# Performance work log

Measured on AMD Instinct MI355X. Metric: run time of the kernel, lower is better.

The kernel has to match this reference:

```python
import jax, jax.numpy as jnp
import numpy as np

B, IN, D1, H1, H2, NC = 16384, 1024, 8, 2048, 1024, 1000
C = IN // D1  # 128 channels, D=8 each
EPS = 1e-5


def _bn(x, g, b):
    # training-mode BatchNorm1d: biased variance over batch dim
    m = jnp.mean(x, axis=0)
    v = jnp.var(x, axis=0)
    return (x - m) * jax.lax.rsqrt(v + EPS) * g + b


def setup_inputs() -> dict:
    key = jax.random.key(0)
    ks = jax.random.split(key, 18)
    f = jax.random.normal
    return {
        "x": f(ks[0], (B, IN), jnp.float32),
        "norm0_g": 1.0 + 0.1 * f(ks[1], (IN,), jnp.float32),
        "norm0_b": 0.1 * f(ks[2], (IN,), jnp.float32),
        "S": f(ks[3], (C, D1, 15), jnp.float32),
        "Hm": f(ks[4], (15, 16), jnp.float32),
        "T": f(ks[5], (C, 15), jnp.float32),
        "LUT": f(ks[6], (C, 16, D1), jnp.float32),
        "W1": 0.02 * f(ks[7], (H1, IN), jnp.float32),
        "b1": 0.02 * f(ks[8], (H1,), jnp.float32),
        "norm1_g": 1.0 + 0.1 * f(ks[9], (H1,), jnp.float32),
        "norm1_b": 0.1 * f(ks[10], (H1,), jnp.float32),
        "W2": 0.02 * f(ks[11], (H2, H1), jnp.float32),
        "b2": 0.02 * f(ks[12], (H2,), jnp.float32),
        "norm2_g": 1.0 + 0.1 * f(ks[13], (H2,), jnp.float32),
        "norm2_b": 0.1 * f(ks[14], (H2,), jnp.float32),
        "W3": 0.02 * f(ks[15], (NC, H2), jnp.float32),
        "b3": 0.02 * f(ks[16], (NC,), jnp.float32),
    }


def reference(x, norm0_g, norm0_b, S, Hm, T, LUT, W1, b1,
              norm1_g, norm1_b, W2, b2, norm2_g, norm2_b, W3, b3):
    h = _bn(x, norm0_g, norm0_b)
    # --- MM block: per-channel small GEMMs + STE sign + STE argmax LUT ---
    xc = h.reshape(-1, C, D1)                          # [B, C, D]
    z = jnp.einsum('bcd,cdk->bck', xc, S) - T - 1e-4   # [B, C, 15]
    t = jnp.tanh(z)
    q = jax.lax.stop_gradient(jnp.sign(z) - t) + t     # STE sign
    logits = jnp.einsum('bck,kj->bcj', q, Hm)          # [B, C, 16]
    one_hot = jax.nn.one_hot(jnp.argmax(logits, axis=-1), 16, dtype=logits.dtype)
    sm = jax.nn.softmax(logits, axis=-1)
    oh_out = jnp.einsum('bck,ckd->bcd', one_hot, LUT)
    sm_out = jnp.einsum('bck,ckd->bcd', sm, LUT)
    v = jax.lax.stop_gradient(oh_out - sm_out) + sm_out  # STE argmax select
    v = v.reshape(-1, C * D1)                           # [B, IN]
    # --- MLP head ---
    h1 = jax.nn.relu(_bn(v @ W1.T + b1, norm1_g, norm1_b))
    h2 = jax.nn.relu(_bn(h1 @ W2.T + b2, norm2_g, norm2_b))
    logits3 = h2 @ W3.T + b3
    return jax.nn.log_softmax(logits3, axis=-1), h1
```

## Files before the change

### kernel.cpp

```cpp
#include <hip/hip_runtime.h>

typedef unsigned short u16;
typedef __attribute__((ext_vector_type(8))) short bf16x8;
typedef __attribute__((ext_vector_type(4))) float f32x4;
typedef __attribute__((ext_vector_type(4))) u16 u16x4;
typedef __attribute__((ext_vector_type(8))) u16 u16x8;

__device__ __forceinline__ u16 f2bf(float f) {
    union { float f; unsigned u; } v; v.f = f;
    unsigned u = v.u;
    unsigned r = (u + 0x7fffu + ((u >> 16) & 1u)) >> 16;
    return (u16)r;
}
__device__ __forceinline__ float bf2f(u16 u) {
    union { unsigned u; float f; } v; v.u = ((unsigned)u) << 16;
    return v.f;
}

__device__ __forceinline__ void gload16(const u16* g, u16* l) {
    __builtin_amdgcn_global_load_lds((const __attribute__((address_space(1))) void*)g,
                                     (__attribute__((address_space(3))) void*)l, 16, 0, 0);
}

#define WAITV(N) asm volatile("s_waitcnt vmcnt(" #N ")" ::: "memory")

__device__ __forceinline__ void sbar() {
    __builtin_amdgcn_sched_barrier(0);
    __builtin_amdgcn_s_barrier();
    __builtin_amdgcn_sched_barrier(0);
}

__device__ __forceinline__ void cvt4(const float* in, u16* out, int i) {
    f32x4 v = *(const f32x4*)(in + (size_t)i * 4);
    u16x4 o;
    o.x = f2bf(v.x); o.y = f2bf(v.y); o.z = f2bf(v.z); o.w = f2bf(v.w);
    *(u16x4*)(out + (size_t)i * 4) = o;
}

__global__ __launch_bounds__(256) void leaf_kernel(
    const float* __restrict__ W1, const float* __restrict__ W2, const float* __restrict__ W3,
    u16* __restrict__ W1b, u16* __restrict__ W2b, u16* __restrict__ W3b,
    const float* __restrict__ x, float* __restrict__ part0) {
    int bid = blockIdx.x;
    if (bid < 5120) {
        int i = bid * 256 + threadIdx.x;
        if (i < 524288) {
            cvt4(W1, W1b, i);
        } else if (i < 1048576) {
            cvt4(W2, W2b, i - 524288);
        } else {
            int j = i - 1048576;
            int e = j * 4;
            int row = e >> 10;
            u16x4 o;
            if (row < 1000) {
                f32x4 v = *(const f32x4*)(W3 + e);
                o.x = f2bf(v.x); o.y = f2bf(v.y); o.z = f2bf(v.z); o.w = f2bf(v.w);
            } else {
                o.x = 0; o.y = 0; o.z = 0; o.w = 0;
            }
            *(u16x4*)(W3b + e) = o;
        }
    } else {
        int by = bid - 5120;
        int col = threadIdx.x * 4;
        long base = (long)by * 32 * 1024 + col;
        f32x4 s = {0.f, 0.f, 0.f, 0.f};
        f32x4 q = {0.f, 0.f, 0.f, 0.f};
        for (int r = 0; r < 32; ++r) {
            f32x4 v = *(const f32x4*)(x + base + (long)r * 1024);
            s.x += v.x; s.y += v.y; s.z += v.z; s.w += v.w;
            q.x = fmaf(v.x, v.x, q.x); q.y = fmaf(v.y, v.y, q.y);
            q.z = fmaf(v.z, v.z, q.z); q.w = fmaf(v.w, v.w, q.w);
        }
        long o = ((long)by * 1024 + col) * 2;
        f32x4 p0 = {s.x, q.x, s.y, q.y};
        f32x4 p1 = {s.z, q.z, s.w, q.w};
        *(f32x4*)(part0 + o) = p0;
        *(f32x4*)(part0 + o + 4) = p1;
    }
}

__global__ __launch_bounds__(256) void col_stats_finalize(
    const float* __restrict__ part, int cols, int nblk, float inv_n,
    const float* __restrict__ g, const float* __restrict__ b, float* __restrict__ ab) {
    __shared__ float red[8][64];
    int cl = threadIdx.x & 31;
    int j = threadIdx.x >> 5;
    int col = blockIdx.x * 32 + cl;
    int per = nblk / 8;
    float s = 0.f, ss = 0.f;
    for (int i = 0; i < per; ++i) {
        long o = ((long)(j * per + i) * cols + col) * 2;
        s += part[o]; ss += part[o + 1];
    }
    red[j][cl * 2] = s;
    red[j][cl * 2 + 1] = ss;
    __syncthreads();
    if (threadIdx.x < 32) {
        int c = blockIdx.x * 32 + threadIdx.x;
        float fs = 0.f, fss = 0.f;
#pragma unroll
        for (int jj = 0; jj < 8; ++jj) {
            fs += red[jj][threadIdx.x * 2];
            fss += red[jj][threadIdx.x * 2 + 1];
        }
        float m = fs * inv_n;
        float var = fss * inv_n - m * m;
        float a = g[c] * rsqrtf(var + 1e-5f);
        ab[c * 2 + 0] = a;
        ab[c * 2 + 1] = b[c] - m * a;
    }
}

__global__ __launch_bounds__(256) void mm_block_kernel(
    const float* __restrict__ x, const float* __restrict__ ab0,
    const float* __restrict__ S, const float* __restrict__ Tt,
    const float* __restrict__ Hm, const float* __restrict__ LUT,
    u16* __restrict__ v) {
    __shared__ float sS[480];
    __shared__ float sT[60];
    __shared__ float sHm[240];
    __shared__ float sLUT[512];
    __shared__ float sAB[64];
    const int t = threadIdx.x;
    const int cb = blockIdx.y * 4;

    for (int i = t; i < 480; i += 256) sS[i] = S[cb * 120 + i];
    for (int i = t; i < 60; i += 256)  sT[i] = Tt[cb * 15 + i];
    for (int i = t; i < 240; i += 256) sHm[i] = Hm[i];
    for (int i = t; i < 512; i += 256) sLUT[i] = LUT[cb * 128 + i];
    for (int i = t; i < 64; i += 256)  sAB[i] = ab0[cb * 16 + i];
    __syncthreads();

    const int row = blockIdx.x * 256 + t;
    const float* xp = x + (size_t)row * 1024 + cb * 8;
    float xr[32];
#pragma unroll
    for (int i = 0; i < 8; ++i) {
        f32x4 v4 = *(const f32x4*)(xp + i * 4);
        xr[i * 4 + 0] = v4.x; xr[i * 4 + 1] = v4.y;
        xr[i * 4 + 2] = v4.z; xr[i * 4 + 3] = v4.w;
    }
    u16 ov[32];
#pragma unroll
    for (int ch = 0; ch < 4; ++ch) {
        float h[8];
#pragma unroll
        for (int d = 0; d < 8; ++d)
            h[d] = xr[ch * 8 + d] * sAB[ch * 16 + d * 2] + sAB[ch * 16 + d * 2 + 1];
        float lg[16];
#pragma unroll
        for (int j = 0; j < 16; ++j) lg[j] = 0.f;
        for (int k = 0; k < 15; ++k) {
            float a = 0.f;
#pragma unroll
            for (int d = 0; d < 8; ++d) a = fmaf(h[d], sS[ch * 120 + d * 15 + k], a);
            float z = (a - sT[ch * 15 + k]) - 1e-4f;
            float q = (z > 0.f) ? 1.f : ((z < 0.f) ? -1.f : 0.f);
#pragma unroll
            for (int j = 0; j < 16; ++j) lg[j] = fmaf(q, sHm[k * 16 + j], lg[j]);
        }
        int jb = 0; float best = lg[0];
#pragma unroll
        for (int j = 1; j < 16; ++j) { if (lg[j] > best) { best = lg[j]; jb = j; } }
#pragma unroll
        for (int d = 0; d < 8; ++d) ov[ch * 8 + d] = f2bf(sLUT[ch * 128 + jb * 8 + d]);
    }
    u16* vp = v + (size_t)row * 1024 + cb * 8;
#pragma unroll
    for (int ch = 0; ch < 4; ++ch)
        *(u16x8*)(vp + ch * 8) = *(u16x8*)&ov[ch * 8];
}

__global__ __launch_bounds__(256) void bn_relu_apply8(
    const u16* __restrict__ y, const float* __restrict__ ab, int cols, int total8,
    float* __restrict__ out_f32, u16* __restrict__ out_b16) {
    int i = blockIdx.x * 256 + threadIdx.x;
    if (i >= total8) return;
    long e = (long)i * 8;
    int col = (int)(e % cols);
    u16x8 yv = *(const u16x8*)(y + e);
    float r[8];
#pragma unroll
    for (int d = 0; d < 8; ++d)
        r[d] = fmaxf(bf2f(yv[d]) * ab[(col + d) * 2] + ab[(col + d) * 2 + 1], 0.f);
    if (out_f32) {
        f32x4 rf0 = {r[0], r[1], r[2], r[3]};
        f32x4 rf1 = {r[4], r[5], r[6], r[7]};
        *(f32x4*)(out_f32 + e) = rf0;
        *(f32x4*)(out_f32 + e + 4) = rf1;
    }
    u16x8 o;
#pragma unroll
    for (int d = 0; d < 8; ++d) o[d] = f2bf(r[d]);
    *(u16x8*)(out_b16 + e) = o;
}

#define MFMA16(a, b, c) __builtin_amdgcn_mfma_f32_16x16x32_bf16(a, b, c, 0, 0, 0)

template <bool STORE_BF16, bool DO_STATS>
__global__ __launch_bounds__(512, 2) void gemm256(
    const u16* __restrict__ A, const u16* __restrict__ Bm, void* __restrict__ Cv,
    const float* __restrict__ bias, float* __restrict__ part,
    int M, int N, int K, int ldc, int ncol) {
    extern __shared__ u16 lds[];
    const int BOFF = 32768;
    const int t = threadIdx.x, lane = t & 63, w = t >> 6;
    const int wr = w >> 2, wc = w & 3;
    const int fr = lane & 15, kg = lane >> 4;
    const int gx = gridDim.x, nwg = gx * gridDim.y;
    const int flat = blockIdx.y * gx + blockIdx.x;
    const int swz = (flat & 7) * (nwg >> 3) + (flat >> 3);
    const int bm = (swz % gx) * 256;
    const int bn = (swz / gx) * 256;
    const int NT = K >> 6;

    const int srow8 = lane >> 3;
    const int scc = (lane & 7) ^ srow8;
    const int L0 = w * 2;
    const u16* gAb = A + ((size_t)bm + L0 * 8 + srow8) * K + scc * 8;
    const u16* gBb = Bm + ((size_t)bn + L0 * 8 + srow8) * K + scc * 8;
    u16* ldsW = lds + L0 * 512 + lane * 8;

    const int s0 = (kg ^ (fr & 7)) * 8;
    const int s1 = s0 ^ 32;
    int rA[4], rB[2];
#pragma unroll
    for (int i = 0; i < 4; ++i) rA[i] = (i * 32 + wr * 16 + fr) * 64;
#pragma unroll
    for (int p = 0; p < 2; ++p) rB[p] = (p * 64 + wc * 16 + fr) * 64;

    f32x4 acc[8][4];
#pragma unroll
    for (int m = 0; m < 8; ++m)
#pragma unroll
        for (int n = 0; n < 4; ++n) acc[m][n] = (f32x4){0.f, 0.f, 0.f, 0.f};

    bf16x8 Ar[8][2], Br[2][2];

#define STG(gp, matOff, d, half, k0)                                          \
    {                                                                         \
        u16* dst_ = ldsW + (matOff) + ((d) * 2 + (half)) * 8192;              \
        const u16* src_ = (gp) + (size_t)((half) * 128) * K + (k0);           \
        gload16(src_, dst_);                                                  \
        gload16(src_ + (size_t)8 * K, dst_ + 512);                            \
    }
#define LDF(off) (*(const bf16x8*)&lds[off])

    STG(gAb, 0, 0, 0, 0);
    STG(gBb, BOFF, 0, 0, 0);
    STG(gAb, 0, 0, 1, 0);
    STG(gBb, BOFF, 0, 1, 0);

#pragma unroll 2
    for (int tt = 0; tt < NT - 1; ++tt) {
        const int d = tt & 1, dn = d ^ 1;
        const int k0n = (tt + 1) << 6;
        const int a0 = (d * 2) * 8192, a1 = (d * 2 + 1) * 8192;
        const int b0 = BOFF + a0, b1 = BOFF + a1;
        WAITV(4); sbar();
        STG(gAb, 0, dn, 0, k0n);
#pragma unroll
        for (int i = 0; i < 4; ++i) { Ar[i][0] = LDF(a0 + rA[i] + s0); Ar[i][1] = LDF(a0 + rA[i] + s1); }
#pragma unroll
        for (int p = 0; p < 2; ++p) { Br[p][0] = LDF(b0 + rB[p] + s0); Br[p][1] = LDF(b0 + rB[p] + s1); }
        __builtin_amdgcn_s_setprio(1);
#pragma unroll
        for (int i = 0; i < 4; ++i)
#pragma unroll
            for (int p = 0; p < 2; ++p) {
                acc[i][p] = MFMA16(Ar[i][0], Br[p][0], acc[i][p]);
                acc[i][p] = MFMA16(Ar[i][1], Br[p][1], acc[i][p]);
            }
        __builtin_amdgcn_s_setprio(0);
        WAITV(4); sbar();
        STG(gBb, BOFF, dn, 0, k0n);
#pragma unroll
        for (int i = 0; i < 4; ++i) { Ar[4 + i][0] = LDF(a1 + rA[i] + s0); Ar[4 + i][1] = LDF(a1 + rA[i] + s1); }
        __builtin_amdgcn_s_setprio(1);
#pragma unroll
        for (int i = 0; i < 4; ++i)
#pragma unroll
            for (int p = 0; p < 2; ++p) {
                acc[4 + i][p] = MFMA16(Ar[4 + i][0], Br[p][0], acc[4 + i][p]);
                acc[4 + i][p] = MFMA16(Ar[4 + i][1], Br[p][1], acc[4 + i][p]);
            }
        __builtin_amdgcn_s_setprio(0);
        WAITV(4); sbar();
        STG(gAb, 0, dn, 1, k0n);
#pragma unroll
        for (int p = 0; p < 2; ++p) { Br[p][0] = LDF(b1 + rB[p] + s0); Br[p][1] = LDF(b1 + rB[p] + s1); }
        __builtin_amdgcn_s_setprio(1);
#pragma unroll
        for (int i = 0; i < 4; ++i)
#pragma unroll
            for (int p = 0; p < 2; ++p) {
                acc[4 + i][2 + p] = MFMA16(Ar[4 + i][0], Br[p][0], acc[4 + i][2 + p]);
                acc[4 + i][2 + p] = MFMA16(Ar[4 + i][1], Br[p][1], acc[4 + i][2 + p]);
            }
        __builtin_amdgcn_s_setprio(0);
        STG(gBb, BOFF, dn, 1, k0n);
        __builtin_amdgcn_s_setprio(1);
#pragma unroll
        for (int i = 0; i < 4; ++i)
#pragma unroll
            for (int p = 0; p < 2; ++p) {
                acc[i][2 + p] = MFMA16(Ar[i][0], Br[p][0], acc[i][2 + p]);
                acc[i][2 + p] = MFMA16(Ar[i][1], Br[p][1], acc[i][2 + p]);
            }
        __builtin_amdgcn_s_setprio(0);
    }
    {
        const int d = (NT - 1) & 1;
        const int a0 = (d * 2) * 8192, a1 = (d * 2 + 1) * 8192;
        const int b0 = BOFF + a0, b1 = BOFF + a1;
        WAITV(4); sbar();
#pragma unroll
        for (int i = 0; i < 4; ++i) { Ar[i][0] = LDF(a0 + rA[i] + s0); Ar[i][1] = LDF(a0 + rA[i] + s1); }
#pragma unroll
        for (int p = 0; p < 2; ++p) { Br[p][0] = LDF(b0 + rB[p] + s0); Br[p][1] = LDF(b0 + rB[p] + s1); }
        __builtin_amdgcn_s_setprio(1);
#pragma unroll
        for (int i = 0; i < 4; ++i)
#pragma unroll
            for (int p = 0; p < 2; ++p) {
                acc[i][p] = MFMA16(Ar[i][0], Br[p][0], acc[i][p]);
                acc[i][p] = MFMA16(Ar[i][1], Br[p][1], acc[i][p]);
            }
        __builtin_amdgcn_s_setprio(0);
        WAITV(2); sbar();
#pragma unroll
        for (int i = 0; i < 4; ++i) { Ar[4 + i][0] = LDF(a1 + rA[i] + s0); Ar[4 + i][1] = LDF(a1 + rA[i] + s1); }
        __builtin_amdgcn_s_setprio(1);
#pragma unroll
        for (int i = 0; i < 4; ++i)
#pragma unroll
            for (int p = 0; p < 2; ++p) {
                acc[4 + i][p] = MFMA16(Ar[4 + i][0], Br[p][0], acc[4 + i][p]);
                acc[4 + i][p] = MFMA16(Ar[4 + i][1], Br[p][1], acc[4 + i][p]);
            }
        __builtin_amdgcn_s_setprio(0);
        WAITV(0); sbar();
#pragma unroll
        for (int p = 0; p < 2; ++p) { Br[p][0] = LDF(b1 + rB[p] + s0); Br[p][1] = LDF(b1 + rB[p] + s1); }
        __builtin_amdgcn_s_setprio(1);
#pragma unroll
        for (int i = 0; i < 4; ++i)
#pragma unroll
            for (int p = 0; p < 2; ++p) {
                acc[4 + i][2 + p] = MFMA16(Ar[4 + i][0], Br[p][0], acc[4 + i][2 + p]);
                acc[4 + i][2 + p] = MFMA16(Ar[4 + i][1], Br[p][1], acc[4 + i][2 + p]);
                acc[i][2 + p] = MFMA16(Ar[i][0], Br[p][0], acc[i][2 + p]);
                acc[i][2 + p] = MFMA16(Ar[i][1], Br[p][1], acc[i][2 + p]);
            }
        __builtin_amdgcn_s_setprio(0);
    }

    const int fq = lane >> 4;
    if (STORE_BF16) {
        u16* C = (u16*)Cv;
        u16* sm = lds;
        const int orow = t >> 4;
        const int ocol = (t & 15) * 16;
#pragma unroll
        for (int m = 0; m < 8; ++m) {
            __syncthreads();
#pragma unroll
            for (int n = 0; n < 4; ++n)
#pragma unroll
                for (int j = 0; j < 4; ++j)
                    sm[(wr * 16 + fq * 4 + j) * 256 + n * 64 + wc * 16 + fr] = f2bf(acc[m][n][j]);
            __syncthreads();
            u16x8 o0 = *(const u16x8*)&sm[orow * 256 + ocol];
            u16x8 o1 = *(const u16x8*)&sm[orow * 256 + ocol + 8];
            u16* cp = C + (size_t)(bm + m * 32 + orow) * ldc + bn + ocol;
            *(u16x8*)cp = o0;
            *(u16x8*)(cp + 8) = o1;
        }
    } else {
#pragma unroll
        for (int m = 0; m < 8; ++m) {
#pragma unroll
            for (int n = 0; n < 4; ++n) {
                int row = bm + m * 32 + wr * 16 + fq * 4;
                int col = bn + n * 64 + wc * 16 + fr;
                if (col < ncol) {
                    float* C = (float*)Cv;
                    float bv = bias ? bias[col] : 0.f;
#pragma unroll
                    for (int j = 0; j < 4; ++j)
                        C[(size_t)(row + j) * ldc + col] = acc[m][n][j] + bv;
                }
            }
        }
    }

    if (DO_STATS) {
        __syncthreads();
        float* smf = (float*)lds;
        float sv[4], qv[4];
#pragma unroll
        for (int n = 0; n < 4; ++n) {
            float s = 0.f, q = 0.f;
#pragma unroll
            for (int m = 0; m < 8; ++m)
#pragma unroll
                for (int j = 0; j < 4; ++j) {
                    float vv = acc[m][n][j];
                    s += vv;
                    q = fmaf(vv, vv, q);
                }
            s += __shfl_xor(s, 16); s += __shfl_xor(s, 32);
            q += __shfl_xor(q, 16); q += __shfl_xor(q, 32);
            sv[n] = s; qv[n] = q;
        }
        if (lane < 16) {
#pragma unroll
            for (int n = 0; n < 4; ++n) {
                smf[(w * 64 + n * 16 + lane) * 2 + 0] = sv[n];
                smf[(w * 64 + n * 16 + lane) * 2 + 1] = qv[n];
            }
        }
        __syncthreads();
        if (t < 256) {
            int n = t >> 6, wcq = (t >> 4) & 3, frq = t & 15;
            int i0 = (wcq * 64 + n * 16 + frq) * 2;
            int i1 = ((4 + wcq) * 64 + n * 16 + frq) * 2;
            long o = ((long)(bm >> 8) * N + bn + t) * 2;
            part[o] = smf[i0] + smf[i1];
            part[o + 1] = smf[i0 + 1] + smf[i1 + 1];
        }
    }
#undef STG
#undef LDF
}

__global__ __launch_bounds__(256) void log_softmax_wave(float* __restrict__ y) {
    const int w = threadIdx.x >> 6;
    const int lane = threadIdx.x & 63;
    float* p = y + ((size_t)blockIdx.x * 4 + w) * 1000;
    const bool has3 = lane < 58;
    f32x4 v0 = ((const f32x4*)p)[lane];
    f32x4 v1 = ((const f32x4*)p)[lane + 64];
    f32x4 v2 = ((const f32x4*)p)[lane + 128];
    f32x4 v3 = has3 ? ((const f32x4*)p)[lane + 192]
                    : (f32x4){-1e30f, -1e30f, -1e30f, -1e30f};
    float m = fmaxf(fmaxf(fmaxf(v0.x, v0.y), fmaxf(v0.z, v0.w)),
                    fmaxf(fmaxf(v1.x, v1.y), fmaxf(v1.z, v1.w)));
    m = fmaxf(m, fmaxf(fmaxf(v2.x, v2.y), fmaxf(v2.z, v2.w)));
    m = fmaxf(m, fmaxf(fmaxf(v3.x, v3.y), fmaxf(v3.z, v3.w)));
#pragma unroll
    for (int d = 32; d > 0; d >>= 1) m = fmaxf(m, __shfl_xor(m, d));
    float sum = expf(v0.x - m) + expf(v0.y - m) + expf(v0.z - m) + expf(v0.w - m)
              + expf(v1.x - m) + expf(v1.y - m) + expf(v1.z - m) + expf(v1.w - m)
              + expf(v2.x - m) + expf(v2.y - m) + expf(v2.z - m) + expf(v2.w - m)
              + expf(v3.x - m) + expf(v3.y - m) + expf(v3.z - m) + expf(v3.w - m);
#pragma unroll
    for (int d = 32; d > 0; d >>= 1) sum += __shfl_xor(sum, d);
    float lse = m + logf(sum);
    v0.x -= lse; v0.y -= lse; v0.z -= lse; v0.w -= lse;
    v1.x -= lse; v1.y -= lse; v1.z -= lse; v1.w -= lse;
    v2.x -= lse; v2.y -= lse; v2.z -= lse; v2.w -= lse;
    ((f32x4*)p)[lane] = v0;
    ((f32x4*)p)[lane + 64] = v1;
    ((f32x4*)p)[lane + 128] = v2;
    if (has3) {
        v3.x -= lse; v3.y -= lse; v3.z -= lse; v3.w -= lse;
        ((f32x4*)p)[lane + 192] = v3;
    }
}

extern "C" void kernel_launch(void* const* d_in, const int* in_sizes, int n_in,
                              void* d_out, int out_size, void* d_ws, size_t ws_size,
                              hipStream_t stream) {
    const float* x   = (const float*)d_in[0];
    const float* n0g = (const float*)d_in[1];
    const float* n0b = (const float*)d_in[2];
    const float* S   = (const float*)d_in[3];
    const float* Hm  = (const float*)d_in[4];
    const float* Tt  = (const float*)d_in[5];
    const float* LUT = (const float*)d_in[6];
    const float* W1  = (const float*)d_in[7];
    const float* n1g = (const float*)d_in[9];
    const float* n1b = (const float*)d_in[10];
    const float* W2  = (const float*)d_in[11];
    const float* n2g = (const float*)d_in[13];
    const float* n2b = (const float*)d_in[14];
    const float* W3  = (const float*)d_in[15];
    const float* b3  = (const float*)d_in[16];

    const int B = 16384, IN = 1024, H1 = 2048, H2 = 1024;
    const int NBY0 = 512;

    hipFuncSetAttribute((const void*)&gemm256<true, true>,
                        hipFuncAttributeMaxDynamicSharedMemorySize, 131072);
    hipFuncSetAttribute((const void*)&gemm256<false, false>,
                        hipFuncAttributeMaxDynamicSharedMemorySize, 131072);

    char* ws = (char*)d_ws;
    size_t off = 0;
    auto alloc = [&](size_t bytes) -> char* {
        char* p = ws + off;
        off += (bytes + 255) & ~(size_t)255;
        return p;
    };
    float* ab0  = (float*)alloc(IN * 2 * sizeof(float));
    float* ab1  = (float*)alloc(H1 * 2 * sizeof(float));
    float* ab2  = (float*)alloc(H2 * 2 * sizeof(float));
    float* part0 = (float*)alloc((size_t)NBY0 * IN * 2 * sizeof(float));
    float* part1 = (float*)alloc((size_t)(B / 256) * H1 * 2 * sizeof(float));
    float* part2 = (float*)alloc((size_t)(B / 256) * H2 * 2 * sizeof(float));
    u16* W1b = (u16*)alloc((size_t)H1 * IN * 2);
    u16* W2b = (u16*)alloc((size_t)H2 * H1 * 2);
    u16* W3b = (u16*)alloc((size_t)1024 * 1024 * 2);
    u16* vb  = (u16*)alloc((size_t)B * IN * 2);
    u16* y1b = (u16*)alloc((size_t)B * H1 * 2);

    float* out0 = (float*)d_out;
    float* out1 = out0 + (size_t)B * 1000;

    leaf_kernel<<<5120 + NBY0, 256, 0, stream>>>(W1, W2, W3, W1b, W2b, W3b, x, part0);

    col_stats_finalize<<<IN / 32, 256, 0, stream>>>(part0, IN, NBY0, 1.f / B, n0g, n0b, ab0);

    mm_block_kernel<<<dim3(B / 256, 32), 256, 0, stream>>>(x, ab0, S, Tt, Hm, LUT, vb);

    gemm256<true, true><<<dim3(B / 256, H1 / 256), 512, 131072, stream>>>(
        vb, W1b, y1b, nullptr, part1, B, H1, IN, H1, H1);

    col_stats_finalize<<<H1 / 32, 256, 0, stream>>>(part1, H1, B / 256, 1.f / B, n1g, n1b, ab1);
    bn_relu_apply8<<<B * H1 / 8 / 256, 256, 0, stream>>>(y1b, ab1, H1, B * H1 / 8, out1, y1b);

    gemm256<true, true><<<dim3(B / 256, H2 / 256), 512, 131072, stream>>>(
        y1b, W2b, vb, nullptr, part2, B, H2, H1, H2, H2);

    col_stats_finalize<<<H2 / 32, 256, 0, stream>>>(part2, H2, B / 256, 1.f / B, n2g, n2b, ab2);
    bn_relu_apply8<<<B * H2 / 8 / 256, 256, 0, stream>>>(vb, ab2, H2, B * H2 / 8, nullptr, vb);

    gemm256<false, false><<<dim3(B / 256, 1024 / 256), 512, 131072, stream>>>(
        vb, W3b, out0, b3, nullptr, B, 1024, H2, 1000, 1000);

    log_softmax_wave<<<B / 4, 256, 0, stream>>>(out0);
}
```

Measured before the change: 360.5 us.

## Overlap fp32 h1 output write with second GEMM via extra writer workgroups

The bn_relu kernel for layer 1 no longer writes the fp32 h1 output. Instead, the layer-2 GEMM launch gets two extra grid rows of workgroups that read the bf16 activations and write them to the fp32 output with nontemporal stores, overlapping this memory-bound write with the compute-bound GEMM. The log-softmax stores also become nontemporal. The trade-off is that h1 is now derived from bf16-rounded values rather than the fp32 result, and the writer traffic competes with the GEMM for memory bandwidth.

```diff
diff --git a/kernel.cpp b/kernel.cpp
--- a/kernel.cpp
+++ b/kernel.cpp
@@ -199,17 +199,31 @@
 
 #define MFMA16(a, b, c) __builtin_amdgcn_mfma_f32_16x16x32_bf16(a, b, c, 0, 0, 0)
 
-template <bool STORE_BF16, bool DO_STATS>
+template <bool STORE_BF16, bool DO_STATS, bool WRITER>
 __global__ __launch_bounds__(512, 2) void gemm256(
     const u16* __restrict__ A, const u16* __restrict__ Bm, void* __restrict__ Cv,
     const float* __restrict__ bias, float* __restrict__ part,
-    int M, int N, int K, int ldc, int ncol) {
+    int M, int N, int K, int ldc, int ncol,
+    const u16* __restrict__ wsrc, float* __restrict__ wdst, long wn4) {
     extern __shared__ u16 lds[];
+    const int t = threadIdx.x;
+    const int gyG = WRITER ? ((int)gridDim.y - 2) : (int)gridDim.y;
+    if (WRITER && (int)blockIdx.y >= gyG) {
+        long wblk = (long)((int)blockIdx.y - gyG) * gridDim.x + blockIdx.x;
+        long tid = wblk * 512 + t;
+        for (long c = tid; c < wn4; c += 65536) {
+            u16x4 v = *(const u16x4*)(wsrc + c * 4);
+            f32x4 o = {bf2f(v.x), bf2f(v.y), bf2f(v.z), bf2f(v.w)};
+            __builtin_nontemporal_store(o, (f32x4*)(wdst + c * 4));
+        }
+        return;
+    }
     const int BOFF = 32768;
-    const int t = threadIdx.x, lane = t & 63, w = t >> 6;
+    const int lane = t & 63, w = t >> 6;
     const int wr = w >> 2, wc = w & 3;
     const int fr = lane & 15, kg = lane >> 4;
-    const int gx = gridDim.x, nwg = gx * gridDim.y;
+    const int gx = gridDim.x;
+    const int nwg = gx * gyG;
     const int flat = blockIdx.y * gx + blockIdx.x;
     const int swz = (flat & 7) * (nwg >> 3) + (flat >> 3);
     const int bm = (swz % gx) * 256;
@@ -462,12 +476,12 @@
     v0.x -= lse; v0.y -= lse; v0.z -= lse; v0.w -= lse;
     v1.x -= lse; v1.y -= lse; v1.z -= lse; v1.w -= lse;
     v2.x -= lse; v2.y -= lse; v2.z -= lse; v2.w -= lse;
-    ((f32x4*)p)[lane] = v0;
-    ((f32x4*)p)[lane + 64] = v1;
-    ((f32x4*)p)[lane + 128] = v2;
+    __builtin_nontemporal_store(v0, &((f32x4*)p)[lane]);
+    __builtin_nontemporal_store(v1, &((f32x4*)p)[lane + 64]);
+    __builtin_nontemporal_store(v2, &((f32x4*)p)[lane + 128]);
     if (has3) {
         v3.x -= lse; v3.y -= lse; v3.z -= lse; v3.w -= lse;
-        ((f32x4*)p)[lane + 192] = v3;
+        __builtin_nontemporal_store(v3, &((f32x4*)p)[lane + 192]);
     }
 }
 
@@ -493,9 +507,11 @@
     const int B = 16384, IN = 1024, H1 = 2048, H2 = 1024;
     const int NBY0 = 512;
 
-    hipFuncSetAttribute((const void*)&gemm256<true, true>,
+    hipFuncSetAttribute((const void*)&gemm256<true, true, false>,
                         hipFuncAttributeMaxDynamicSharedMemorySize, 131072);
-    hipFuncSetAttribute((const void*)&gemm256<false, false>,
+    hipFuncSetAttribute((const void*)&gemm256<true, true, true>,
+                        hipFuncAttributeMaxDynamicSharedMemorySize, 131072);
+    hipFuncSetAttribute((const void*)&gemm256<false, false, false>,
                         hipFuncAttributeMaxDynamicSharedMemorySize, 131072);
 
     char* ws = (char*)d_ws;
@@ -526,20 +542,21 @@
 
     mm_block_kernel<<<dim3(B / 256, 32), 256, 0, stream>>>(x, ab0, S, Tt, Hm, LUT, vb);
 
-    gemm256<true, true><<<dim3(B / 256, H1 / 256), 512, 131072, stream>>>(
-        vb, W1b, y1b, nullptr, part1, B, H1, IN, H1, H1);
+    gemm256<true, true, false><<<dim3(B / 256, H1 / 256), 512, 131072, stream>>>(
+        vb, W1b, y1b, nullptr, part1, B, H1, IN, H1, H1, nullptr, nullptr, 0);
 
     col_stats_finalize<<<H1 / 32, 256, 0, stream>>>(part1, H1, B / 256, 1.f / B, n1g, n1b, ab1);
-    bn_relu_apply8<<<B * H1 / 8 / 256, 256, 0, stream>>>(y1b, ab1, H1, B * H1 / 8, out1, y1b);
-
-    gemm256<true, true><<<dim3(B / 256, H2 / 256), 512, 131072, stream>>>(
-        y1b, W2b, vb, nullptr, part2, B, H2, H1, H2, H2);
+    bn_relu_apply8<<<B * H1 / 8 / 256, 256, 0, stream>>>(y1b, ab1, H1, B * H1 / 8, nullptr, y1b);
+
+    gemm256<true, true, true><<<dim3(B / 256, H2 / 256 + 2), 512, 131072, stream>>>(
+        y1b, W2b, vb, nullptr, part2, B, H2, H1, H2, H2,
+        y1b, out1, (long)B * H1 / 4);
 
     col_stats_finalize<<<H2 / 32, 256, 0, stream>>>(part2, H2, B / 256, 1.f / B, n2g, n2b, ab2);
     bn_relu_apply8<<<B * H2 / 8 / 256, 256, 0, stream>>>(vb, ab2, H2, B * H2 / 8, nullptr, vb);
 
-    gemm256<false, false><<<dim3(B / 256, 1024 / 256), 512, 131072, stream>>>(
-        vb, W3b, out0, b3, nullptr, B, 1024, H2, 1000, 1000);
+    gemm256<false, false, false><<<dim3(B / 256, 1024 / 256), 512, 131072, stream>>>(
+        vb, W3b, out0, b3, nullptr, B, 1024, H2, 1000, 1000, nullptr, nullptr, 0);
 
     log_softmax_wave<<<B / 4, 256, 0, stream>>>(out0);
 }
```

After: 357.8 us (median of 2 runs). Within noise of the previous version (-0.7%).
